# Kernel tuning notes

Measured on AMD Instinct MI355X. Metric: run time of the kernel, lower is better.

The kernel has to match this reference:

```python
import jax, jax.numpy as jnp
import numpy as np

D_MODEL = 1024
NUM_HEADS = 16
D_K = D_MODEL // NUM_HEADS


def setup_inputs() -> dict:
    key = jax.random.key(0)
    ks = jax.random.split(key, 9)
    s = 1.0 / np.sqrt(D_MODEL)
    x = jax.random.normal(ks[0], (2, 2048, D_MODEL), dtype=jnp.float32)
    mk = lambda k: jax.random.uniform(k, (D_MODEL, D_MODEL), jnp.float32, -s, s)
    mb = lambda k: jax.random.uniform(k, (D_MODEL,), jnp.float32, -s, s)
    return {
        "x": x,
        "Wq": mk(ks[1]), "bq": mb(ks[2]),
        "Wk": mk(ks[3]), "bk": mb(ks[4]),
        "Wv": mk(ks[5]), "bv": mb(ks[6]),
        "Wo": mk(ks[7]), "bo": mb(ks[8]),
    }


def _attn(x, Wq, bq, Wk, bk, Wv, bv, Wo, bo):
    B, S, _ = x.shape
    # torch Linear: y = x @ W.T + b; weights stored [out, in]
    def proj(W, b):
        y = jnp.einsum('bsd,ed->bse', x, W) + b
        return y.reshape(B, S, NUM_HEADS, D_K).transpose(0, 2, 1, 3)  # [B,H,S,Dk]
    Q = proj(Wq, bq)
    K = proj(Wk, bk)
    V = proj(Wv, bv)
    scale = 1.0 / np.sqrt(D_K).astype(np.float32)
    scores = jnp.einsum('bhqd,bhkd->bhqk', Q, K) * scale  # [B,H,S,S]
    # FAITHFUL to source: softmax over dim=1 (the HEAD axis), a quirk of the original code
    attn = jax.nn.softmax(scores, axis=1)
    context = jnp.einsum('bhqk,bhkd->bhqd', attn, V)  # [B,H,S,Dk]
    context = context.transpose(0, 2, 1, 3).reshape(B, S, D_MODEL)
    return jnp.einsum('bsd,ed->bse', context, Wo) + bo


def reference(x, Wq, bq, Wk, bk, Wv, bv, Wo, bo):
    return _attn(x, Wq, bq, Wk, bk, Wv, bv, Wo, bo)
```

## Files before the change

kernel.cpp:

```cpp
#include <hip/hip_runtime.h>


#define D_MODEL 1024
#define NH 16
#define DKH 64
#define SEQ 2048
#define NB 2
#define NTOK (NB * SEQ)
#define OSC 0.180336880f

typedef float f32x4 __attribute__((ext_vector_type(4)));
typedef short bf16x8 __attribute__((ext_vector_type(8)));

static __device__ __forceinline__ unsigned short f2bf(float x) {
    union { float f; unsigned int u; } c; c.f = x;
    unsigned int r = (c.u + 0x7FFFu + ((c.u >> 16) & 1u)) >> 16;
    return (unsigned short)r;
}
static __device__ __forceinline__ unsigned int pack2(float a, float b) {
    return (unsigned int)f2bf(a) | ((unsigned int)f2bf(b) << 16);
}
static __device__ __forceinline__ unsigned int pack2rn(float a, float b) {
    union { float f; unsigned int u; } ca, cb; ca.f = a; cb.f = b;
    return __builtin_amdgcn_perm(cb.u + 0x8000u, ca.u + 0x8000u, 0x07060302u);
}
static __device__ __forceinline__ unsigned int pack2tr(float a, float b) {
    union { float f; unsigned int u; } ca, cb; ca.f = a; cb.f = b;
    return __builtin_amdgcn_perm(cb.u, ca.u, 0x07060302u);
}
static __device__ __forceinline__ float bflo(unsigned int u) {
    union { unsigned int x; float f; } c; c.x = u << 16; return c.f;
}
static __device__ __forceinline__ float bfhi(unsigned int u) {
    union { unsigned int x; float f; } c; c.x = u & 0xFFFF0000u; return c.f;
}
static __device__ __forceinline__ f32x4 mfma16(uint4 a, uint4 b, f32x4 c) {
    return __builtin_amdgcn_mfma_f32_16x16x32_bf16(
        __builtin_bit_cast(bf16x8, a), __builtin_bit_cast(bf16x8, b), c, 0, 0, 0);
}
static __device__ __forceinline__ void gl_lds16(const unsigned short* g, unsigned short* l) {
    __builtin_amdgcn_global_load_lds(
        (const __attribute__((address_space(1))) unsigned int*)g,
        (__attribute__((address_space(3))) unsigned int*)l, 16, 0, 0);
}
static __device__ __forceinline__ int fsw(int row) {
    return (row & 7) ^ ((row >> 2) & 7);
}

__global__ __launch_bounds__(256) void cvt4(
    const float* __restrict__ x, const float* __restrict__ w0,
    const float* __restrict__ w1, const float* __restrict__ w2,
    unsigned short* __restrict__ xb, unsigned short* __restrict__ Wb3)
{
    int bid = blockIdx.x;
    const float* src;
    unsigned short* dst;
    size_t i;
    if (bid < 2048) {
        src = x; dst = xb;
        i = ((size_t)bid * 256 + threadIdx.x) * 8;
    } else {
        int r = bid - 2048;
        int sel = r >> 9, blk = r & 511;
        src = (sel == 0) ? w0 : (sel == 1) ? w1 : w2;
        dst = Wb3 + (size_t)sel * D_MODEL * D_MODEL;
        i = ((size_t)blk * 256 + threadIdx.x) * 8;
    }
    float4 a = *(const float4*)(src + i);
    float4 b = *(const float4*)(src + i + 4);
    uint4 p = { pack2(a.x, a.y), pack2(a.z, a.w), pack2(b.x, b.y), pack2(b.z, b.w) };
    *(uint4*)(dst + i) = p;
}

__global__ __launch_bounds__(256) void cvt_k(const float* __restrict__ x,
                                             unsigned short* __restrict__ xb)
{
    size_t i = ((size_t)blockIdx.x * 256 + threadIdx.x) * 8;
    float4 a = *(const float4*)(x + i);
    float4 b = *(const float4*)(x + i + 4);
    uint4 p = { pack2(a.x, a.y), pack2(a.z, a.w), pack2(b.x, b.y), pack2(b.z, b.w) };
    *(uint4*)(xb + i) = p;
}

__global__ __launch_bounds__(256) void gemm_qkv4(
    const unsigned short* __restrict__ A, const unsigned short* __restrict__ Wb3,
    const float* __restrict__ bq, const float* __restrict__ bk,
    const float* __restrict__ bv, unsigned short* __restrict__ Qh,
    unsigned short* __restrict__ Kh, unsigned short* __restrict__ Vt)
{
    __shared__ unsigned short lds[12288];
    unsigned short* lA = lds;
    unsigned short* lB = lds + 8192;
    const int tid = threadIdx.x;
    const int wv = tid >> 6, lane = tid & 63, quad = lane >> 4, lm = lane & 15;
    const int wm = wv >> 1, wn = wv & 1;
    const int bid = blockIdx.x;
    const int xcd = bid & 7, slot = bid >> 3;
    const int mg = xcd >> 1, sg = xcd & 1;
    const int mtile = mg * 8 + (slot & 7);
    const int sn = sg * 24 + (slot >> 3);
    const int sel = sn >> 4;
    const int ncol = sn & 15;
    const int m0 = mtile * 128, n0 = ncol * 64;
    const int sub = lane >> 3, chl = (lane & 7) ^ sub;
    const unsigned short* Wb = Wb3 + (size_t)sel * D_MODEL * D_MODEL;
    const float* bias = (sel == 0) ? bq : (sel == 1) ? bk : bv;
    const float osc = (sel == 0) ? OSC : 1.0f;

    f32x4 acc[4][2] = {};

    for (int k0 = 0; k0 < D_MODEL; k0 += 64) {
        __syncthreads();
#pragma unroll
        for (int j = 0; j < 4; ++j) {
            int rbase = wv * 32 + j * 8;
            gl_lds16(A + (size_t)(m0 + rbase + sub) * D_MODEL + k0 + chl * 8,
                     &lA[rbase * 64]);
        }
#pragma unroll
        for (int j = 0; j < 2; ++j) {
            int rbase = wv * 16 + j * 8;
            gl_lds16(Wb + (size_t)(n0 + rbase + sub) * D_MODEL + k0 + chl * 8,
                     &lB[rbase * 64]);
        }
        __syncthreads();
#pragma unroll
        for (int ks = 0; ks < 2; ++ks) {
            uint4 af[4];
#pragma unroll
            for (int mt = 0; mt < 4; ++mt)
                af[mt] = *(const uint4*)&lA[(wm * 64 + mt * 16 + lm) * 64 +
                                            ((ks * 4 + quad) ^ (lm & 7)) * 8];
#pragma unroll
            for (int nt = 0; nt < 2; ++nt) {
                uint4 bf = *(const uint4*)&lB[(wn * 32 + nt * 16 + lm) * 64 +
                                              ((ks * 4 + quad) ^ (lm & 7)) * 8];
#pragma unroll
                for (int mt = 0; mt < 4; ++mt)
                    acc[mt][nt] = mfma16(af[mt], bf, acc[mt][nt]);
            }
        }
    }

    if (sel < 2) {
        unsigned short* out = (sel == 0) ? Qh : Kh;
#pragma unroll
        for (int nt = 0; nt < 2; ++nt) {
            int n = n0 + wn * 32 + nt * 16 + lm;
            float bvv = bias[n];
            int h = n >> 6, d = n & 63;
#pragma unroll
            for (int mt = 0; mt < 4; ++mt)
#pragma unroll
                for (int r = 0; r < 4; ++r) {
                    int m = m0 + wm * 64 + mt * 16 + quad * 4 + r;
                    int b = m >> 11, q = m & 2047;
                    out[((size_t)(b * NH + h) * SEQ + q) * DKH + d] =
                        f2bf((acc[mt][nt][r] + bvv) * osc);
                }
        }
    } else {
        __syncthreads();
        unsigned short* T = lds;
#pragma unroll
        for (int nt = 0; nt < 2; ++nt) {
            int nl = wn * 32 + nt * 16 + lm;
            float bvv = bias[n0 + nl];
#pragma unroll
            for (int mt = 0; mt < 4; ++mt) {
                int ml = wm * 64 + mt * 16 + quad * 4;
                uint2 p = { pack2rn(acc[mt][nt][0] + bvv, acc[mt][nt][1] + bvv),
                            pack2rn(acc[mt][nt][2] + bvv, acc[mt][nt][3] + bvv) };
                *(uint2*)&T[nl * 128 + ml] = p;
            }
        }
        __syncthreads();
        int row = tid >> 2, seg = tid & 3;
        int b = m0 >> 11, s0 = m0 & 2047;
        unsigned short* dst = Vt + ((size_t)(b * D_MODEL) + n0 + row) * SEQ + s0 + seg * 32;
        const unsigned short* src = &T[row * 128 + seg * 32];
#pragma unroll
        for (int i = 0; i < 4; ++i)
            *(uint4*)(dst + i * 8) = *(const uint4*)(src + i * 8);
    }
}

template <int KS>
__global__ __launch_bounds__(256) void psum_wo(
    const unsigned short* __restrict__ OP, unsigned short* __restrict__ OPs,
    const float* __restrict__ Wo, unsigned short* __restrict__ WoB)
{
    int bid = blockIdx.x;
    if (bid >= 2048) {
        size_t i = ((size_t)(bid - 2048) * 256 + threadIdx.x) * 8;
        float4 a = *(const float4*)(Wo + i);
        float4 b = *(const float4*)(Wo + i + 4);
        uint4 p = { pack2(a.x, a.y), pack2(a.z, a.w), pack2(b.x, b.y), pack2(b.z, b.w) };
        *(uint4*)(WoB + i) = p;
        return;
    }
    const size_t M = (size_t)NTOK * D_MODEL;
    size_t i = ((size_t)bid * 256 + threadIdx.x) * 8;
    uint4 a = *(const uint4*)(OP + i);
    float lo0 = bflo(a.x), hi0 = bfhi(a.x), lo1 = bflo(a.y), hi1 = bfhi(a.y);
    float lo2 = bflo(a.z), hi2 = bfhi(a.z), lo3 = bflo(a.w), hi3 = bfhi(a.w);
#pragma unroll
    for (int p = 1; p < KS; ++p) {
        uint4 u = *(const uint4*)(OP + p * M + i);
        lo0 += bflo(u.x); hi0 += bfhi(u.x); lo1 += bflo(u.y); hi1 += bfhi(u.y);
        lo2 += bflo(u.z); hi2 += bfhi(u.z); lo3 += bflo(u.w); hi3 += bfhi(u.w);
    }
    uint4 o = { pack2(lo0, hi0), pack2(lo1, hi1), pack2(lo2, hi2), pack2(lo3, hi3) };
    *(uint4*)(OPs + i) = o;
}

__global__ __launch_bounds__(256) void gemm_osum3(
    const unsigned short* __restrict__ OPs, const unsigned short* __restrict__ WoB,
    const float* __restrict__ bias, float* __restrict__ out)
{
    __shared__ unsigned short lds[2][12288];
    const int tid = threadIdx.x;
    const int wv = tid >> 6, lane = tid & 63, quad = lane >> 4, lm = lane & 15;
    const int wm = wv >> 1, wn = wv & 1;
    const int bid = blockIdx.x;
    const int xcd = bid & 7, slot = bid >> 3;
    const int mg = xcd >> 1, ng = xcd & 1;
    const int mtile = mg * 8 + (slot & 7);
    const int ncol = ng * 8 + (slot >> 3);
    const int m0 = mtile * 128, n0 = ncol * 64;
    const int sub = lane >> 3, chl = (lane & 7) ^ sub;
    const int b = m0 >> 11, q0 = m0 & 2047;

    f32x4 acc[4][2] = {};

    auto stage = [&](int buf, int k0) {
        const int h = k0 >> 6;
        const unsigned short* Ab = OPs + ((size_t)(b * NH + h) * SEQ + q0) * DKH;
        unsigned short* lA = lds[buf];
        unsigned short* lB = lds[buf] + 8192;
#pragma unroll
        for (int j = 0; j < 4; ++j) {
            int rbase = wv * 32 + j * 8;
            gl_lds16(Ab + (size_t)(rbase + sub) * DKH + chl * 8, &lA[rbase * 64]);
        }
#pragma unroll
        for (int j = 0; j < 2; ++j) {
            int rbase = wv * 16 + j * 8;
            gl_lds16(WoB + (size_t)(n0 + rbase + sub) * D_MODEL + k0 + chl * 8,
                     &lB[rbase * 64]);
        }
    };

    stage(0, 0);
    __syncthreads();

    for (int k0 = 0; k0 < D_MODEL; k0 += 64) {
        const int cur = (k0 >> 6) & 1;
        if (k0 + 64 < D_MODEL)
            stage(cur ^ 1, k0 + 64);
        const unsigned short* lA = lds[cur];
        const unsigned short* lB = lds[cur] + 8192;
#pragma unroll
        for (int ks = 0; ks < 2; ++ks) {
            uint4 af[4];
#pragma unroll
            for (int mt = 0; mt < 4; ++mt)
                af[mt] = *(const uint4*)&lA[(wm * 64 + mt * 16 + lm) * 64 +
                                            ((ks * 4 + quad) ^ (lm & 7)) * 8];
#pragma unroll
            for (int nt = 0; nt < 2; ++nt) {
                uint4 bf = *(const uint4*)&lB[(wn * 32 + nt * 16 + lm) * 64 +
                                              ((ks * 4 + quad) ^ (lm & 7)) * 8];
#pragma unroll
                for (int mt = 0; mt < 4; ++mt)
                    acc[mt][nt] = mfma16(af[mt], bf, acc[mt][nt]);
            }
        }
        __syncthreads();
    }
#pragma unroll
    for (int nt = 0; nt < 2; ++nt) {
        int n = n0 + wn * 32 + nt * 16 + lm;
        float bv = bias[n];
#pragma unroll
        for (int mt = 0; mt < 4; ++mt)
#pragma unroll
            for (int r = 0; r < 4; ++r) {
                int m = m0 + wm * 64 + mt * 16 + quad * 4 + r;
                out[(size_t)m * D_MODEL + n] = acc[mt][nt][r] + bv;
            }
    }
}

__global__ __launch_bounds__(256) void zker2(
    const unsigned short* __restrict__ Qh, const unsigned short* __restrict__ Kh,
    unsigned short* __restrict__ rz)
{
    __shared__ unsigned short lK[2][128 * 64];
    const int tid = threadIdx.x;
    const int wv = tid >> 6, lane = tid & 63, quad = lane >> 4, lm = lane & 15;
    const int lid = blockIdx.x;
    const int xcd = lid & 7, slot = lid >> 3;
    const int qb = slot & 15, col = xcd * 4 + (slot >> 4);
    const int b = col >> 4, kb = col & 15;
    const int q0 = qb * 128, k0 = kb * 128;
    const int srow = tid >> 3, sc = tid & 7;

    f32x4 z[2][8] = {};

    auto stagek = [&](int buf, int hh) {
        const size_t kbase = ((size_t)(b * NH + hh) * SEQ + k0) * DKH;
#pragma unroll
        for (int j = 0; j < 4; ++j) {
            int row = j * 32 + srow;
            int g = sc ^ fsw(row);
            gl_lds16(Kh + kbase + (size_t)row * 64 + g * 8,
                     &lK[buf][(j * 32 + wv * 8) * 64]);
        }
    };
    auto loadq = [&](uint4 (&bqr)[2][2], int hh) {
#pragma unroll
        for (int qs = 0; qs < 2; ++qs) {
            const unsigned short* qp = Qh +
                ((size_t)(b * NH + hh) * SEQ + q0 + wv * 32 + qs * 16 + lm) * DKH + quad * 8;
            bqr[qs][0] = *(const uint4*)qp;
            bqr[qs][1] = *(const uint4*)(qp + 32);
        }
    };

    uint4 bq[2][2];
    stagek(0, 0);
    loadq(bq, 0);
    __syncthreads();

    for (int h = 0; h < NH; ++h) {
        const int cur = h & 1;
        uint4 bqn[2][2];
        if (h + 1 < NH) {
            stagek(cur ^ 1, h + 1);
            loadq(bqn, h + 1);
        }
        const unsigned short* cK = lK[cur];
#pragma unroll
        for (int kt = 0; kt < 8; ++kt) {
            int krow = kt * 16 + lm;
            uint4 a0 = *(const uint4*)&cK[krow * 64 + ((quad) ^ fsw(krow)) * 8];
            uint4 a1 = *(const uint4*)&cK[krow * 64 + ((4 + quad) ^ fsw(krow)) * 8];
#pragma unroll
            for (int qs = 0; qs < 2; ++qs) {
                f32x4 sf = {0.f, 0.f, 0.f, 0.f};
                __builtin_amdgcn_s_setprio(1);
                sf = mfma16(a0, bq[qs][0], sf);
                sf = mfma16(a1, bq[qs][1], sf);
                __builtin_amdgcn_s_setprio(0);
#pragma unroll
                for (int r = 0; r < 4; ++r)
                    z[qs][kt][r] += __builtin_amdgcn_exp2f(sf[r]);
            }
        }
        __syncthreads();
        if (h + 1 < NH) {
#pragma unroll
            for (int qs = 0; qs < 2; ++qs) {
                bq[qs][0] = bqn[qs][0];
                bq[qs][1] = bqn[qs][1];
            }
        }
    }
#pragma unroll
    for (int qs = 0; qs < 2; ++qs) {
        int q = q0 + wv * 32 + qs * 16 + lm;
#pragma unroll
        for (int kt = 0; kt < 8; ++kt) {
            int k = k0 + kt * 16 + quad * 4;
            float l0 = __builtin_amdgcn_logf(z[qs][kt][0]);
            float l1 = __builtin_amdgcn_logf(z[qs][kt][1]);
            float l2 = __builtin_amdgcn_logf(z[qs][kt][2]);
            float l3 = __builtin_amdgcn_logf(z[qs][kt][3]);
            uint2 st = { pack2rn(-l0, -l1), pack2rn(-l2, -l3) };
            *(uint2*)(rz + (size_t)(b * SEQ + q) * SEQ + k) = st;
        }
    }
}

template <int KS>
__global__ __launch_bounds__(256) void attn4(
    const unsigned short* __restrict__ Qh, const unsigned short* __restrict__ Kh,
    const unsigned short* __restrict__ Vt, const unsigned short* __restrict__ rz,
    unsigned short* __restrict__ OP)
{
    __shared__ unsigned short lK[64 * 64];
    __shared__ unsigned short lV[64 * 64];
    const int tid = threadIdx.x;
    const int wv = tid >> 6, lane = tid & 63, quad = lane >> 4, lm = lane & 15;
    const int lid = blockIdx.x;
    int b, h, ksl, qb;
    if constexpr (KS == 4) {
        const int xcd = lid & 7, slot = lid >> 3;
        b = xcd >> 2; ksl = xcd & 3;
        qb = slot >> 4; h = slot & 15;
    } else {
        const int xcd = lid & 7, slot = lid >> 3;
        qb = slot & 15;
        const int combo = xcd * (4 * KS) + (slot >> 4);
        const int bh = combo / KS; ksl = combo % KS;
        b = bh >> 4; h = bh & 15;
    }
    const int q0 = qb * 128;
    const int NIT = (SEQ / KS) / 64;
    const int kbeg = ksl * (SEQ / KS);
    const int q0w = q0 + wv * 32;
    const size_t hb = (size_t)(b * NH + h) * SEQ;
    const int srow = tid >> 3, sc = tid & 7;

    uint4 qf[2][2];
#pragma unroll
    for (int qs = 0; qs < 2; ++qs)
#pragma unroll
        for (int ks = 0; ks < 2; ++ks)
            qf[qs][ks] = *(const uint4*)(Qh + (hb + q0w + qs * 16 + lm) * DKH +
                                         ks * 32 + quad * 8);

    const int perm = ((lm >> 2) * 8) + (lm & 3);
    f32x4 oa[4][2] = {};

    for (int kt = 0; kt < NIT; ++kt) {
        const int kbase = kbeg + kt * 64;
        __syncthreads();
#pragma unroll
        for (int j = 0; j < 2; ++j) {
            int row = j * 32 + srow;
            int g = sc ^ fsw(row);
            gl_lds16(Kh + (hb + kbase + row) * DKH + g * 8,
                     &lK[(j * 32 + wv * 8) * 64]);
        }
#pragma unroll
        for (int j = 0; j < 2; ++j) {
            int row = j * 32 + srow;
            int g = sc ^ fsw(row);
            gl_lds16(Vt + ((size_t)(b * D_MODEL) + h * DKH + row) * SEQ + kbase + g * 8,
                     &lV[(j * 32 + wv * 8) * 64]);
        }
        uint4 rv[2][2];
#pragma unroll
        for (int qs = 0; qs < 2; ++qs)
#pragma unroll
            for (int gr = 0; gr < 2; ++gr)
                rv[gr][qs] = *(const uint4*)(rz +
                    (size_t)(b * SEQ + q0w + qs * 16 + lm) * SEQ +
                    kbase + gr * 32 + quad * 8);
        __syncthreads();

#pragma unroll
        for (int gr = 0; gr < 2; ++gr) {
            f32x4 sf[2][2];
#pragma unroll
            for (int qs = 0; qs < 2; ++qs) {
                uint4 rq = rv[gr][qs];
                sf[0][qs][0] = bflo(rq.x); sf[0][qs][1] = bfhi(rq.x);
                sf[0][qs][2] = bflo(rq.y); sf[0][qs][3] = bfhi(rq.y);
                sf[1][qs][0] = bflo(rq.z); sf[1][qs][1] = bfhi(rq.z);
                sf[1][qs][2] = bflo(rq.w); sf[1][qs][3] = bfhi(rq.w);
            }
#pragma unroll
            for (int sel = 0; sel < 2; ++sel) {
                int key = gr * 32 + perm + sel * 4;
#pragma unroll
                for (int ks = 0; ks < 2; ++ks) {
                    uint4 kfv = *(const uint4*)&lK[key * 64 +
                                                   ((ks * 4 + quad) ^ fsw(key)) * 8];
                    sf[sel][0] = mfma16(kfv, qf[0][ks], sf[sel][0]);
                    sf[sel][1] = mfma16(kfv, qf[1][ks], sf[sel][1]);
                }
            }
            uint4 pk[2];
#pragma unroll
            for (int qs = 0; qs < 2; ++qs) {
                float p00 = __builtin_amdgcn_exp2f(sf[0][qs][0]);
                float p01 = __builtin_amdgcn_exp2f(sf[0][qs][1]);
                float p02 = __builtin_amdgcn_exp2f(sf[0][qs][2]);
                float p03 = __builtin_amdgcn_exp2f(sf[0][qs][3]);
                float p10 = __builtin_amdgcn_exp2f(sf[1][qs][0]);
                float p11 = __builtin_amdgcn_exp2f(sf[1][qs][1]);
                float p12 = __builtin_amdgcn_exp2f(sf[1][qs][2]);
                float p13 = __builtin_amdgcn_exp2f(sf[1][qs][3]);
                pk[qs].x = pack2tr(p00, p01);
                pk[qs].y = pack2tr(p02, p03);
                pk[qs].z = pack2tr(p10, p11);
                pk[qs].w = pack2tr(p12, p13);
            }
#pragma unroll
            for (int ct = 0; ct < 4; ++ct) {
                int vrow = ct * 16 + lm;
                uint4 vfv = *(const uint4*)&lV[vrow * 64 +
                                               ((gr * 4 + quad) ^ fsw(vrow)) * 8];
                oa[ct][0] = mfma16(vfv, pk[0], oa[ct][0]);
                oa[ct][1] = mfma16(vfv, pk[1], oa[ct][1]);
            }
        }
    }

    unsigned short* op = OP + (size_t)ksl * NTOK * D_MODEL;
#pragma unroll
    for (int ct = 0; ct < 4; ++ct)
#pragma unroll
        for (int qs = 0; qs < 2; ++qs) {
            uint2 st = { pack2rn(oa[ct][qs][0], oa[ct][qs][1]),
                         pack2rn(oa[ct][qs][2], oa[ct][qs][3]) };
            *(uint2*)(op + (hb + q0w + qs * 16 + lm) * DKH + ct * 16 + quad * 4) = st;
        }
}

extern "C" void kernel_launch(void* const* d_in, const int* in_sizes, int n_in,
                              void* d_out, int out_size, void* d_ws, size_t ws_size,
                              hipStream_t stream)
{
    const float* x  = (const float*)d_in[0];
    const float* Wq = (const float*)d_in[1];
    const float* bq = (const float*)d_in[2];
    const float* Wk = (const float*)d_in[3];
    const float* bk = (const float*)d_in[4];
    const float* Wv = (const float*)d_in[5];
    const float* bv = (const float*)d_in[6];
    const float* Wo = (const float*)d_in[7];
    const float* bo = (const float*)d_in[8];
    float* out = (float*)d_out;

    const size_t M  = (size_t)NTOK * D_MODEL;
    const size_t RZ = (size_t)NB * SEQ * SEQ;
    unsigned short* ws = (unsigned short*)d_ws;
    unsigned short* rzb = ws;
    unsigned short* xb  = ws;
    unsigned short* Qh  = ws + RZ;
    unsigned short* Kh  = Qh + M;
    unsigned short* Vt  = Kh + M;
    unsigned short* OP  = Vt + M;
    unsigned short* Wb3 = OP;
    unsigned short* OPs = Qh;
    unsigned short* WoB = rzb;

    const size_t need4 = (RZ + 3 * M + 4 * M) * sizeof(unsigned short);
    const size_t need2 = (RZ + 3 * M + 2 * M) * sizeof(unsigned short);
    const int KS = (ws_size >= need4) ? 4 : (ws_size >= need2) ? 2 : 1;

    cvt4<<<3584, 256, 0, stream>>>(x, Wq, Wk, Wv, xb, Wb3);
    gemm_qkv4<<<1536, 256, 0, stream>>>(xb, Wb3, bq, bk, bv, Qh, Kh, Vt);
    zker2<<<512, 256, 0, stream>>>(Qh, Kh, rzb);
    if (KS == 4)      attn4<4><<<2048, 256, 0, stream>>>(Qh, Kh, Vt, rzb, OP);
    else if (KS == 2) attn4<2><<<1024, 256, 0, stream>>>(Qh, Kh, Vt, rzb, OP);
    else              attn4<1><<<512, 256, 0, stream>>>(Qh, Kh, Vt, rzb, OP);
    if (KS == 4)      psum_wo<4><<<2560, 256, 0, stream>>>(OP, OPs, Wo, WoB);
    else if (KS == 2) psum_wo<2><<<2560, 256, 0, stream>>>(OP, OPs, Wo, WoB);
    else {
        cvt_k<<<512, 256, 0, stream>>>(Wo, WoB);
        OPs = OP;
    }
    gemm_osum3<<<512, 256, 0, stream>>>(OPs, WoB, bo, out);
}
```

Baseline: 238.9 us.

## Fuse split-K partial-sum reduction into output projection GEMM A-tile staging

Removes the separate psum_wo kernel that reduced the KS attention partial outputs into a bf16 buffer. The output GEMM now loads all KS partials for its A tile into registers, sums them, and writes the folded tile to LDS while the MFMAs for the current tile run. Wo is converted by cvt_k on its own. This saves one launch and the write and reread of the summed buffer. In exchange, each of the 8 column-tile blocks sharing a row tile re-reads all KS partials, adds register pressure from the ra array, and replaces async global-to-LDS loads with synchronous ones.

```diff
diff --git a/kernel.cpp b/kernel.cpp
--- a/kernel.cpp
+++ b/kernel.cpp
@@ -186,36 +186,8 @@
 }
 
 template <int KS>
-__global__ __launch_bounds__(256) void psum_wo(
-    const unsigned short* __restrict__ OP, unsigned short* __restrict__ OPs,
-    const float* __restrict__ Wo, unsigned short* __restrict__ WoB)
-{
-    int bid = blockIdx.x;
-    if (bid >= 2048) {
-        size_t i = ((size_t)(bid - 2048) * 256 + threadIdx.x) * 8;
-        float4 a = *(const float4*)(Wo + i);
-        float4 b = *(const float4*)(Wo + i + 4);
-        uint4 p = { pack2(a.x, a.y), pack2(a.z, a.w), pack2(b.x, b.y), pack2(b.z, b.w) };
-        *(uint4*)(WoB + i) = p;
-        return;
-    }
-    const size_t M = (size_t)NTOK * D_MODEL;
-    size_t i = ((size_t)bid * 256 + threadIdx.x) * 8;
-    uint4 a = *(const uint4*)(OP + i);
-    float lo0 = bflo(a.x), hi0 = bfhi(a.x), lo1 = bflo(a.y), hi1 = bfhi(a.y);
-    float lo2 = bflo(a.z), hi2 = bfhi(a.z), lo3 = bflo(a.w), hi3 = bfhi(a.w);
-#pragma unroll
-    for (int p = 1; p < KS; ++p) {
-        uint4 u = *(const uint4*)(OP + p * M + i);
-        lo0 += bflo(u.x); hi0 += bfhi(u.x); lo1 += bflo(u.y); hi1 += bfhi(u.y);
-        lo2 += bflo(u.z); hi2 += bfhi(u.z); lo3 += bflo(u.w); hi3 += bfhi(u.w);
-    }
-    uint4 o = { pack2(lo0, hi0), pack2(lo1, hi1), pack2(lo2, hi2), pack2(lo3, hi3) };
-    *(uint4*)(OPs + i) = o;
-}
-
-__global__ __launch_bounds__(256) void gemm_osum3(
-    const unsigned short* __restrict__ OPs, const unsigned short* __restrict__ WoB,
+__global__ __launch_bounds__(256) void gemm_osum4(
+    const unsigned short* __restrict__ OP, const unsigned short* __restrict__ WoB,
     const float* __restrict__ bias, float* __restrict__ out)
 {
     __shared__ unsigned short lds[2][12288];
@@ -230,19 +202,48 @@
     const int m0 = mtile * 128, n0 = ncol * 64;
     const int sub = lane >> 3, chl = (lane & 7) ^ sub;
     const int b = m0 >> 11, q0 = m0 & 2047;
+    const size_t M = (size_t)NTOK * D_MODEL;
 
     f32x4 acc[4][2] = {};
-
-    auto stage = [&](int buf, int k0) {
+    uint4 ra[4][KS];
+
+    auto loadA = [&](int k0) {
         const int h = k0 >> 6;
-        const unsigned short* Ab = OPs + ((size_t)(b * NH + h) * SEQ + q0) * DKH;
+        const size_t abase = ((size_t)(b * NH + h) * SEQ + q0) * DKH;
+#pragma unroll
+        for (int j = 0; j < 4; ++j) {
+            const unsigned short* src =
+                OP + abase + (size_t)(wv * 32 + j * 8 + sub) * DKH + chl * 8;
+#pragma unroll
+            for (int p = 0; p < KS; ++p)
+                ra[j][p] = *(const uint4*)(src + (size_t)p * M);
+        }
+    };
+    auto foldA = [&](int buf) {
         unsigned short* lA = lds[buf];
+#pragma unroll
+        for (int j = 0; j < 4; ++j) {
+            uint4 o;
+            if constexpr (KS == 1) {
+                o = ra[j][0];
+            } else {
+                uint4 a = ra[j][0];
+                float lo0 = bflo(a.x), hi0 = bfhi(a.x), lo1 = bflo(a.y), hi1 = bfhi(a.y);
+                float lo2 = bflo(a.z), hi2 = bfhi(a.z), lo3 = bflo(a.w), hi3 = bfhi(a.w);
+#pragma unroll
+                for (int p = 1; p < KS; ++p) {
+                    uint4 u = ra[j][p];
+                    lo0 += bflo(u.x); hi0 += bfhi(u.x); lo1 += bflo(u.y); hi1 += bfhi(u.y);
+                    lo2 += bflo(u.z); hi2 += bfhi(u.z); lo3 += bflo(u.w); hi3 += bfhi(u.w);
+                }
+                o = (uint4){ pack2(lo0, hi0), pack2(lo1, hi1),
+                             pack2(lo2, hi2), pack2(lo3, hi3) };
+            }
+            *(uint4*)&lA[(wv * 32 + j * 8) * 64 + lane * 8] = o;
+        }
+    };
+    auto stageB = [&](int buf, int k0) {
         unsigned short* lB = lds[buf] + 8192;
-#pragma unroll
-        for (int j = 0; j < 4; ++j) {
-            int rbase = wv * 32 + j * 8;
-            gl_lds16(Ab + (size_t)(rbase + sub) * DKH + chl * 8, &lA[rbase * 64]);
-        }
 #pragma unroll
         for (int j = 0; j < 2; ++j) {
             int rbase = wv * 16 + j * 8;
@@ -251,13 +252,18 @@
         }
     };
 
-    stage(0, 0);
+    loadA(0);
+    stageB(0, 0);
+    foldA(0);
     __syncthreads();
 
     for (int k0 = 0; k0 < D_MODEL; k0 += 64) {
         const int cur = (k0 >> 6) & 1;
-        if (k0 + 64 < D_MODEL)
-            stage(cur ^ 1, k0 + 64);
+        const bool more = (k0 + 64 < D_MODEL);
+        if (more) {
+            loadA(k0 + 64);
+            stageB(cur ^ 1, k0 + 64);
+        }
         const unsigned short* lA = lds[cur];
         const unsigned short* lB = lds[cur] + 8192;
 #pragma unroll
@@ -276,6 +282,7 @@
                     acc[mt][nt] = mfma16(af[mt], bf, acc[mt][nt]);
             }
         }
+        if (more) foldA(cur ^ 1);
         __syncthreads();
     }
 #pragma unroll
@@ -536,7 +543,6 @@
     unsigned short* Vt  = Kh + M;
     unsigned short* OP  = Vt + M;
     unsigned short* Wb3 = OP;
-    unsigned short* OPs = Qh;
     unsigned short* WoB = rzb;
 
     const size_t need4 = (RZ + 3 * M + 4 * M) * sizeof(unsigned short);
@@ -549,11 +555,8 @@
     if (KS == 4)      attn4<4><<<2048, 256, 0, stream>>>(Qh, Kh, Vt, rzb, OP);
     else if (KS == 2) attn4<2><<<1024, 256, 0, stream>>>(Qh, Kh, Vt, rzb, OP);
     else              attn4<1><<<512, 256, 0, stream>>>(Qh, Kh, Vt, rzb, OP);
-    if (KS == 4)      psum_wo<4><<<2560, 256, 0, stream>>>(OP, OPs, Wo, WoB);
-    else if (KS == 2) psum_wo<2><<<2560, 256, 0, stream>>>(OP, OPs, Wo, WoB);
-    else {
-        cvt_k<<<512, 256, 0, stream>>>(Wo, WoB);
-        OPs = OP;
-    }
-    gemm_osum3<<<512, 256, 0, stream>>>(OPs, WoB, bo, out);
-}
+    cvt_k<<<512, 256, 0, stream>>>(Wo, WoB);
+    if (KS == 4)      gemm_osum4<4><<<512, 256, 0, stream>>>(OP, WoB, bo, out);
+    else if (KS == 2) gemm_osum4<2><<<512, 256, 0, stream>>>(OP, WoB, bo, out);
+    else              gemm_osum4<1><<<512, 256, 0, stream>>>(OP, WoB, bo, out);
+}
```

After: 255.4 us. +6.9%, slower.
